# Performance work log

Hardware: AMD Instinct MI355X
Metric: run time of the kernel (lower is better)

The kernel has to match this reference:

```python
import jax, jax.numpy as jnp
import numpy as np

N = 200000   # nodes
E = 6400000  # directed edges (avg degree 32)
F = 128      # num_features
C = 16       # num_classes
H1, H2, H3 = 4, 4, 2  # hardcoded GCN hidden dims from the source


def setup_inputs():
    key = jax.random.key(0)
    ks = jax.random.split(key, 10)
    x = jax.random.normal(ks[0], (N, F), dtype=jnp.float32)
    edge_index = jax.random.randint(ks[1], (2, E), 0, N, dtype=jnp.int32)
    def lin(k, fin, fout):
        return jax.random.normal(k, (fin, fout), dtype=jnp.float32) / np.sqrt(fin).astype(np.float32)
    return {
        "x": x,
        "W1": lin(ks[2], F, H1),  "b1": jnp.zeros((H1,), jnp.float32),
        "W2": lin(ks[3], H1, H2), "b2": jnp.zeros((H2,), jnp.float32),
        "W3": lin(ks[4], H2, H3), "b3": jnp.zeros((H3,), jnp.float32),
        "Wc": lin(ks[5], H3, C),  "bc": jnp.zeros((C,), jnp.float32),
        "edge_index": edge_index,
    }


def _gcn_conv(h, W, b, src, dst, norm, n):
    # PyG GCNConv: linear first, then normalized scatter-add aggregation, then bias
    h = h @ W                                   # [n, fout]
    msg = h[src] * norm[:, None]                # gather + per-edge scale
    out = jax.ops.segment_sum(msg, dst, num_segments=n)
    return out + b


def reference(x, W1, b1, W2, b2, W3, b3, Wc, bc, edge_index):
    n = x.shape[0]
    # add self-loops (GCNConv default add_self_loops=True)
    loop = jnp.arange(n, dtype=edge_index.dtype)
    src = jnp.concatenate([edge_index[0], loop])
    dst = jnp.concatenate([edge_index[1], loop])
    # symmetric degree normalization: norm_e = deg(dst)^-1/2 * deg(src)^-1/2
    deg = jax.ops.segment_sum(jnp.ones(src.shape[0], dtype=x.dtype), dst, num_segments=n)
    dinv = jnp.where(deg > 0, jax.lax.rsqrt(deg), jnp.zeros_like(deg))
    norm = dinv[src] * dinv[dst]
    h = jnp.tanh(_gcn_conv(x, W1, b1, src, dst, norm, n))
    h = jnp.tanh(_gcn_conv(h, W2, b2, src, dst, norm, n))
    h = jnp.tanh(_gcn_conv(h, W3, b3, src, dst, norm, n))
    out = h @ Wc + bc
    return (out, h)
```

## Files before the change

kernel.cpp:

```cpp
#include <hip/hip_runtime.h>
#include <math.h>


#define NR 500
#define RNG 400
#define CAP 16384
#define HB 1024
#define EPT 8
#define EPB (HB * EPT)
#define SCAP 14336
#define Q 8
#define LROWS 32
#define LPAD 133


__global__ void k_initcur(int* __restrict__ cursor) {
    int t = blockIdx.x * blockDim.x + threadIdx.x;
    if (t < NR) cursor[t * 16] = t * CAP;
}

__global__ __launch_bounds__(HB) void k_build(const int* __restrict__ src,
                                              const int* __restrict__ dst,
                                              int* __restrict__ cursor,
                                              int* __restrict__ csrp, int e) {
    __shared__ int hist[NR];
    __shared__ int scn[HB];
    __shared__ int start[NR + 1];
    __shared__ int gbase[NR];
    __shared__ int cur[NR];
    __shared__ int buf[EPB];

    int t = threadIdx.x;
    for (int i = t; i < NR; i += HB) hist[i] = 0;
    __syncthreads();

    int ds[EPT], sr[EPT];
    int base = blockIdx.x * EPB;
#pragma unroll
    for (int k = 0; k < 2; k++) {
        int idx = base + k * HB * 4 + t * 4;
        if (idx + 3 < e) {
            int4 d4 = *(const int4*)(dst + idx);
            int4 s4 = *(const int4*)(src + idx);
            ds[4 * k + 0] = d4.x; ds[4 * k + 1] = d4.y; ds[4 * k + 2] = d4.z; ds[4 * k + 3] = d4.w;
            sr[4 * k + 0] = s4.x; sr[4 * k + 1] = s4.y; sr[4 * k + 2] = s4.z; sr[4 * k + 3] = s4.w;
        } else {
#pragma unroll
            for (int j = 0; j < 4; j++) {
                int i2 = idx + j;
                if (i2 < e) { ds[4 * k + j] = dst[i2]; sr[4 * k + j] = src[i2]; }
                else ds[4 * k + j] = -1;
            }
        }
    }
#pragma unroll
    for (int k = 0; k < EPT; k++)
        if (ds[k] >= 0) atomicAdd(&hist[ds[k] / RNG], 1);
    __syncthreads();

    scn[t] = (t < NR) ? hist[t] : 0;
    __syncthreads();
    for (int off = 1; off < HB; off <<= 1) {
        int add = (t >= off) ? scn[t - off] : 0;
        __syncthreads();
        scn[t] += add;
        __syncthreads();
    }
    if (t < NR) {
        int c = hist[t];
        int st = scn[t] - c;
        start[t] = st;
        cur[t] = st;
        gbase[t] = c ? atomicAdd(&cursor[t * 16], c) : 0;
    }
    if (t == 0) start[NR] = scn[NR - 1];
    __syncthreads();

#pragma unroll
    for (int k = 0; k < EPT; k++) {
        if (ds[k] >= 0) {
            int bin = ds[k] / RNG;
            int p = atomicAdd(&cur[bin], 1);
            buf[p] = (sr[k] << 9) | (ds[k] - bin * RNG);
        }
    }
    __syncthreads();

    int total = start[NR];
    for (int j = t; j < total; j += HB) {
        int lo = 0, hi = NR;
        while (hi - lo > 1) {
            int mid = (lo + hi) >> 1;
            if (start[mid] <= j) lo = mid; else hi = mid;
        }
        int g = gbase[lo] + (j - start[lo]);
        if (g < (lo + 1) * CAP) csrp[g] = buf[j];
    }
}


__global__ __launch_bounds__(1024) void k_sortbin(int* __restrict__ csrp,
                                                  const int* __restrict__ cursor,
                                                  float* __restrict__ dinv, int n) {
    __shared__ int deg[RNG];
    __shared__ int off[RNG];
    __shared__ int cur[RNG];
    __shared__ int sbuf[SCAP];
    int t = threadIdx.x, b = blockIdx.x;
    int s0 = b * CAP;
    int cnt = cursor[b * 16] - s0;
    if (cnt < 0) cnt = 0; if (cnt > CAP) cnt = CAP;

    for (int i = t; i < RNG; i += 1024) deg[i] = 0;
    __syncthreads();
    for (int j = t; j < cnt; j += 1024)
        atomicAdd(&deg[csrp[s0 + j] & 511], 1);
    __syncthreads();

    if (t < RNG) off[t] = deg[t];
    __syncthreads();
    for (int d = 1; d < RNG; d <<= 1) {
        int u = 0;
        if (t < RNG && t >= d) u = off[t - d];
        __syncthreads();
        if (t < RNG) off[t] += u;
        __syncthreads();
    }
    if (t < RNG) cur[t] = off[t] - deg[t];
    __syncthreads();

    for (int j = t; j < cnt; j += 1024) {
        int p = csrp[s0 + j];
        int r = atomicAdd(&cur[p & 511], 1);
        if (r < SCAP) sbuf[r] = p;
    }
    __syncthreads();
    int lim = (cnt < SCAP) ? cnt : SCAP;
    for (int j = t; j < lim; j += 1024)
        csrp[s0 + j] = sbuf[j];

    int basen = b * RNG;
    for (int i = t; i < RNG; i += 1024) {
        int node = basen + i;
        if (node < n) dinv[node] = rsqrtf(1.0f + (float)deg[i]);
    }
}


__global__ __launch_bounds__(256) void k_linear1(const float* __restrict__ x,
                                                 const float* __restrict__ W1,
                                                 const float* __restrict__ dinv,
                                                 float4* __restrict__ g1, int n) {
    __shared__ float xs[LROWS * LPAD];
    int t = threadIdx.x;
    int q = t & 7, r = t >> 3;
    int row0 = blockIdx.x * LROWS;

    float4 w[16];
#pragma unroll
    for (int i = 0; i < 16; i++) w[i] = ((const float4*)W1)[q * 16 + i];

    const float4* xg = (const float4*)(x + (size_t)row0 * 128);
    int maxI = (n - row0) * 32;
#pragma unroll
    for (int k = 0; k < 4; k++) {
        int idx = t + k * 256;
        if (idx < maxI) {
            float4 v = xg[idx];
            int rr = idx >> 5, cc = (idx & 31) << 2;
            *(float4*)&xs[rr * LPAD + cc] = v;
        }
    }
    __syncthreads();

    float p0 = 0.f, p1 = 0.f, p2 = 0.f, p3 = 0.f;
    const float* xr = &xs[r * LPAD + q * 16];
#pragma unroll
    for (int j = 0; j < 4; j++) {
        float4 xv = *(const float4*)(xr + 4 * j);
        float4 wa = w[4 * j + 0], wb = w[4 * j + 1], wc = w[4 * j + 2], wd = w[4 * j + 3];
        p0 += xv.x * wa.x + xv.y * wb.x + xv.z * wc.x + xv.w * wd.x;
        p1 += xv.x * wa.y + xv.y * wb.y + xv.z * wc.y + xv.w * wd.y;
        p2 += xv.x * wa.z + xv.y * wb.z + xv.z * wc.z + xv.w * wd.z;
        p3 += xv.x * wa.w + xv.y * wb.w + xv.z * wc.w + xv.w * wd.w;
    }
#pragma unroll
    for (int off = 1; off < 8; off <<= 1) {
        p0 += __shfl_xor(p0, off, 64);
        p1 += __shfl_xor(p1, off, 64);
        p2 += __shfl_xor(p2, off, 64);
        p3 += __shfl_xor(p3, off, 64);
    }
    int row = row0 + r;
    if (q == 0 && row < n) {
        float dv = dinv[row];
        g1[row] = make_float4(dv * p0, dv * p1, dv * p2, dv * p3);
    }
}


#define PUSH4() { qd[qc * 256 + t] = cd; \
    qv[(qc * 4 + 0) * 256 + t] = a0; qv[(qc * 4 + 1) * 256 + t] = a1; \
    qv[(qc * 4 + 2) * 256 + t] = a2; qv[(qc * 4 + 3) * 256 + t] = a3; qc++; }
#define EDGE4(di, gv) { int d_ = (di) & 511; \
    if (d_ != cd) { if (cd >= 0) PUSH4(); cd = d_; a0 = gv.x; a1 = gv.y; a2 = gv.z; a3 = gv.w; } \
    else { a0 += gv.x; a1 += gv.y; a2 += gv.z; a3 += gv.w; } }
#define FLUSH4() { for (int q = 0; q < Q; q++) { if (q < qc) { int dd = qd[q * 256 + t]; \
    atomicAdd(&acc[dd * 5 + 0], qv[(q * 4 + 0) * 256 + t]); \
    atomicAdd(&acc[dd * 5 + 1], qv[(q * 4 + 1) * 256 + t]); \
    atomicAdd(&acc[dd * 5 + 2], qv[(q * 4 + 2) * 256 + t]); \
    atomicAdd(&acc[dd * 5 + 3], qv[(q * 4 + 3) * 256 + t]); } } qc = 0; }

#define EDGELOOP4() \
    int s0 = b * CAP; \
    int cnt = cursor[b * 16] - s0; if (cnt < 0) cnt = 0; if (cnt > CAP) cnt = CAP; \
    int per = (((cnt + 255) >> 8) + 3) & ~3; \
    int lo = s0 + t * per; \
    int hi = lo + per; int eE = s0 + cnt; if (hi > eE) hi = eE; \
    int cd = -1; float a0 = 0, a1 = 0, a2 = 0, a3 = 0; \
    int qc = 0; \
    for (int j = lo; j < hi; j += 4) { \
        int4 p = *(const int4*)(csrp + j); \
        int m = hi - j; \
        int i1 = (m > 1) ? p.y : p.x; \
        int i2 = (m > 2) ? p.z : p.x; \
        int i3 = (m > 3) ? p.w : p.x; \
        float4 g0 = gin[(unsigned)p.x >> 9]; \
        float4 g1 = gin[(unsigned)i1 >> 9]; \
        float4 g2 = gin[(unsigned)i2 >> 9]; \
        float4 g3 = gin[(unsigned)i3 >> 9]; \
        EDGE4(p.x, g0); \
        if (m > 1) EDGE4(i1, g1); \
        if (m > 2) EDGE4(i2, g2); \
        if (m > 3) EDGE4(i3, g3); \
        if (__any(qc >= Q - 3)) FLUSH4(); \
    } \
    if (cd >= 0) PUSH4(); \
    FLUSH4(); \
    __syncthreads();

__global__ __launch_bounds__(256) void k_bagg44s(const int* __restrict__ csrp,
                                                 const int* __restrict__ cursor,
                                                 const float* __restrict__ dinv,
                                                 const float4* __restrict__ gin,
                                                 float4* __restrict__ gout,
                                                 const float* __restrict__ W,
                                                 const float* __restrict__ bv, int n) {
    __shared__ float acc[RNG * 5];
    __shared__ float qv[Q * 4 * 256];
    __shared__ int   qd[Q * 256];
    int t = threadIdx.x, b = blockIdx.x;
    for (int i = t; i < RNG * 5; i += 256) acc[i] = 0.0f;
    __syncthreads();
    EDGELOOP4();
    int basen = b * RNG;
    for (int i = t; i < RNG; i += 256) {
        int node = basen + i;
        if (node >= n) continue;
        float4 gs = gin[node];
        float dv = dinv[node];
        float t0 = tanhf(dv * (gs.x + acc[i * 5 + 0]) + bv[0]);
        float t1 = tanhf(dv * (gs.y + acc[i * 5 + 1]) + bv[1]);
        float t2 = tanhf(dv * (gs.z + acc[i * 5 + 2]) + bv[2]);
        float t3 = tanhf(dv * (gs.w + acc[i * 5 + 3]) + bv[3]);
        float4 o;
        o.x = dv * (t0 * W[0] + t1 * W[4] + t2 * W[8]  + t3 * W[12]);
        o.y = dv * (t0 * W[1] + t1 * W[5] + t2 * W[9]  + t3 * W[13]);
        o.z = dv * (t0 * W[2] + t1 * W[6] + t2 * W[10] + t3 * W[14]);
        o.w = dv * (t0 * W[3] + t1 * W[7] + t2 * W[11] + t3 * W[15]);
        gout[node] = o;
    }
}

__global__ __launch_bounds__(256) void k_bagg42s(const int* __restrict__ csrp,
                                                 const int* __restrict__ cursor,
                                                 const float* __restrict__ dinv,
                                                 const float4* __restrict__ gin,
                                                 float2* __restrict__ gout,
                                                 const float* __restrict__ W,
                                                 const float* __restrict__ bv, int n) {
    __shared__ float acc[RNG * 5];
    __shared__ float qv[Q * 4 * 256];
    __shared__ int   qd[Q * 256];
    int t = threadIdx.x, b = blockIdx.x;
    for (int i = t; i < RNG * 5; i += 256) acc[i] = 0.0f;
    __syncthreads();
    EDGELOOP4();
    int basen = b * RNG;
    for (int i = t; i < RNG; i += 256) {
        int node = basen + i;
        if (node >= n) continue;
        float4 gs = gin[node];
        float dv = dinv[node];
        float t0 = tanhf(dv * (gs.x + acc[i * 5 + 0]) + bv[0]);
        float t1 = tanhf(dv * (gs.y + acc[i * 5 + 1]) + bv[1]);
        float t2 = tanhf(dv * (gs.z + acc[i * 5 + 2]) + bv[2]);
        float t3 = tanhf(dv * (gs.w + acc[i * 5 + 3]) + bv[3]);
        float h0 = t0 * W[0] + t1 * W[2] + t2 * W[4] + t3 * W[6];
        float h1 = t0 * W[1] + t1 * W[3] + t2 * W[5] + t3 * W[7];
        gout[node] = make_float2(dv * h0, dv * h1);
    }
}

#define PUSH2() { qd[qc * 256 + t] = cd; \
    qv[(qc * 2 + 0) * 256 + t] = a0; qv[(qc * 2 + 1) * 256 + t] = a1; qc++; }
#define EDGE2(di, gv) { int d_ = (di) & 511; \
    if (d_ != cd) { if (cd >= 0) PUSH2(); cd = d_; a0 = gv.x; a1 = gv.y; } \
    else { a0 += gv.x; a1 += gv.y; } }
#define FLUSH2() { for (int q = 0; q < Q; q++) { if (q < qc) { int dd = qd[q * 256 + t]; \
    atomicAdd(&acc[dd * 3 + 0], qv[(q * 2 + 0) * 256 + t]); \
    atomicAdd(&acc[dd * 3 + 1], qv[(q * 2 + 1) * 256 + t]); } } qc = 0; }

__global__ __launch_bounds__(256) void k_bagg2outs(const int* __restrict__ csrp,
                                                   const int* __restrict__ cursor,
                                                   const float* __restrict__ dinv,
                                                   const float2* __restrict__ gin,
                                                   const float* __restrict__ b3,
                                                   const float* __restrict__ Wc,
                                                   const float* __restrict__ bc,
                                                   float* __restrict__ out,
                                                   float2* __restrict__ hout, int n) {
    __shared__ float acc[RNG * 3];
    __shared__ float qv[Q * 2 * 256];
    __shared__ int   qd[Q * 256];
    int t = threadIdx.x, b = blockIdx.x;
    for (int i = t; i < RNG * 3; i += 256) acc[i] = 0.0f;
    __syncthreads();
    int s0 = b * CAP;
    int cnt = cursor[b * 16] - s0; if (cnt < 0) cnt = 0; if (cnt > CAP) cnt = CAP;
    int per = (((cnt + 255) >> 8) + 3) & ~3;
    int lo = s0 + t * per;
    int hi = lo + per; int eE = s0 + cnt; if (hi > eE) hi = eE;
    int cd = -1; float a0 = 0, a1 = 0;
    int qc = 0;
    for (int j = lo; j < hi; j += 4) {
        int4 p = *(const int4*)(csrp + j);
        int m = hi - j;
        int i1 = (m > 1) ? p.y : p.x;
        int i2 = (m > 2) ? p.z : p.x;
        int i3 = (m > 3) ? p.w : p.x;
        float2 g0 = gin[(unsigned)p.x >> 9];
        float2 g1 = gin[(unsigned)i1 >> 9];
        float2 g2 = gin[(unsigned)i2 >> 9];
        float2 g3 = gin[(unsigned)i3 >> 9];
        EDGE2(p.x, g0);
        if (m > 1) EDGE2(i1, g1);
        if (m > 2) EDGE2(i2, g2);
        if (m > 3) EDGE2(i3, g3);
        if (__any(qc >= Q - 3)) FLUSH2();
    }
    if (cd >= 0) PUSH2();
    FLUSH2();
    __syncthreads();
    int basen = b * RNG;
    for (int i = t; i < RNG; i += 256) {
        int node = basen + i;
        if (node >= n) continue;
        float2 gs = gin[node];
        float dv = dinv[node];
        float t0 = tanhf(dv * (gs.x + acc[i * 3 + 0]) + b3[0]);
        float t1 = tanhf(dv * (gs.y + acc[i * 3 + 1]) + b3[1]);
        hout[node] = make_float2(t0, t1);
        float4* o = (float4*)(out + (size_t)node * 16);
#pragma unroll
        for (int q = 0; q < 4; q++) {
            float4 v;
            v.x = t0 * Wc[4 * q + 0] + t1 * Wc[16 + 4 * q + 0] + bc[4 * q + 0];
            v.y = t0 * Wc[4 * q + 1] + t1 * Wc[16 + 4 * q + 1] + bc[4 * q + 1];
            v.z = t0 * Wc[4 * q + 2] + t1 * Wc[16 + 4 * q + 2] + bc[4 * q + 2];
            v.w = t0 * Wc[4 * q + 3] + t1 * Wc[16 + 4 * q + 3] + bc[4 * q + 3];
            o[q] = v;
        }
    }
}


__global__ void k_count(const int* __restrict__ dst, int* __restrict__ cnt, int e) {
    int i = blockIdx.x * blockDim.x + threadIdx.x;
    if (i < e) atomicAdd(&cnt[dst[i]], 1);
}

__global__ void k_dinv_i(const int* __restrict__ cnt, float* __restrict__ dinv, int n) {
    int i = blockIdx.x * blockDim.x + threadIdx.x;
    if (i < n) dinv[i] = rsqrtf(1.0f + (float)cnt[i]);
}

__global__ void f_linear1(const float* __restrict__ x, const float* __restrict__ W1,
                          const float* __restrict__ dinv,
                          float* __restrict__ h, float* __restrict__ agg, int n) {
    int lane = threadIdx.x & 63;
    int wave = blockIdx.x * (blockDim.x >> 6) + (threadIdx.x >> 6);
    int nwaves = gridDim.x * (blockDim.x >> 6);
    float4 w0 = ((const float4*)W1)[2 * lane];
    float4 w1 = ((const float4*)W1)[2 * lane + 1];
    for (int row = wave; row < n; row += nwaves) {
        float2 xv = ((const float2*)(x + (size_t)row * 128))[lane];
        float p0 = xv.x * w0.x + xv.y * w1.x;
        float p1 = xv.x * w0.y + xv.y * w1.y;
        float p2 = xv.x * w0.z + xv.y * w1.z;
        float p3 = xv.x * w0.w + xv.y * w1.w;
#pragma unroll
        for (int off = 32; off; off >>= 1) {
            p0 += __shfl_xor(p0, off, 64);
            p1 += __shfl_xor(p1, off, 64);
            p2 += __shfl_xor(p2, off, 64);
            p3 += __shfl_xor(p3, off, 64);
        }
        if (lane == 0) {
            float dv = dinv[row]; float dv2 = dv * dv;
            ((float4*)h)[row] = make_float4(p0, p1, p2, p3);
            ((float4*)agg)[row] = make_float4(dv2 * p0, dv2 * p1, dv2 * p2, dv2 * p3);
        }
    }
}

__global__ void k_edge4(const int* __restrict__ src, const int* __restrict__ dst,
                        const float* __restrict__ dinv, const float* __restrict__ h,
                        float* __restrict__ agg, int e) {
    int i = blockIdx.x * blockDim.x + threadIdx.x;
    if (i >= e) return;
    int s = src[i], d = dst[i];
    float w = dinv[s] * dinv[d];
    float4 hv = ((const float4*)h)[s];
    float* a = agg + 4 * (size_t)d;
    unsafeAtomicAdd(a + 0, w * hv.x);
    unsafeAtomicAdd(a + 1, w * hv.y);
    unsafeAtomicAdd(a + 2, w * hv.z);
    unsafeAtomicAdd(a + 3, w * hv.w);
}

__global__ void k_edge2(const int* __restrict__ src, const int* __restrict__ dst,
                        const float* __restrict__ dinv, const float* __restrict__ h,
                        float* __restrict__ agg, int e) {
    int i = blockIdx.x * blockDim.x + threadIdx.x;
    if (i >= e) return;
    int s = src[i], d = dst[i];
    float w = dinv[s] * dinv[d];
    float2 hv = ((const float2*)h)[s];
    float* a = agg + 2 * (size_t)d;
    unsafeAtomicAdd(a + 0, w * hv.x);
    unsafeAtomicAdd(a + 1, w * hv.y);
}

__global__ void k_fin44(float* __restrict__ h, float* __restrict__ agg,
                        const float* __restrict__ dinv,
                        const float* __restrict__ W, const float* __restrict__ b, int n) {
    int i = blockIdx.x * blockDim.x + threadIdx.x;
    if (i >= n) return;
    float4 a = ((const float4*)agg)[i];
    float t0 = tanhf(a.x + b[0]);
    float t1 = tanhf(a.y + b[1]);
    float t2 = tanhf(a.z + b[2]);
    float t3 = tanhf(a.w + b[3]);
    float hn[4];
#pragma unroll
    for (int k = 0; k < 4; k++)
        hn[k] = t0 * W[k] + t1 * W[4 + k] + t2 * W[8 + k] + t3 * W[12 + k];
    float dv = dinv[i], dv2 = dv * dv;
    ((float4*)h)[i] = make_float4(hn[0], hn[1], hn[2], hn[3]);
    ((float4*)agg)[i] = make_float4(dv2 * hn[0], dv2 * hn[1], dv2 * hn[2], dv2 * hn[3]);
}

__global__ void k_fin42(const float* __restrict__ agg, float* __restrict__ h3,
                        float* __restrict__ agg3, const float* __restrict__ dinv,
                        const float* __restrict__ W, const float* __restrict__ b, int n) {
    int i = blockIdx.x * blockDim.x + threadIdx.x;
    if (i >= n) return;
    float4 a = ((const float4*)agg)[i];
    float t0 = tanhf(a.x + b[0]);
    float t1 = tanhf(a.y + b[1]);
    float t2 = tanhf(a.z + b[2]);
    float t3 = tanhf(a.w + b[3]);
    float h0 = t0 * W[0] + t1 * W[2] + t2 * W[4] + t3 * W[6];
    float h1 = t0 * W[1] + t1 * W[3] + t2 * W[5] + t3 * W[7];
    float dv = dinv[i], dv2 = dv * dv;
    ((float2*)h3)[i] = make_float2(h0, h1);
    ((float2*)agg3)[i] = make_float2(dv2 * h0, dv2 * h1);
}

__global__ void k_final_old(const float* __restrict__ agg3,
                            const float* __restrict__ Wc, const float* __restrict__ b3,
                            const float* __restrict__ bc,
                            float* __restrict__ out, float* __restrict__ hout, int n) {
    int i = blockIdx.x * blockDim.x + threadIdx.x;
    if (i >= n) return;
    float2 a = ((const float2*)agg3)[i];
    float t0 = tanhf(a.x + b3[0]);
    float t1 = tanhf(a.y + b3[1]);
    ((float2*)hout)[i] = make_float2(t0, t1);
    float4* o = (float4*)(out + (size_t)i * 16);
#pragma unroll
    for (int q = 0; q < 4; q++) {
        float4 v;
        v.x = t0 * Wc[4 * q + 0] + t1 * Wc[16 + 4 * q + 0] + bc[4 * q + 0];
        v.y = t0 * Wc[4 * q + 1] + t1 * Wc[16 + 4 * q + 1] + bc[4 * q + 1];
        v.z = t0 * Wc[4 * q + 2] + t1 * Wc[16 + 4 * q + 2] + bc[4 * q + 2];
        v.w = t0 * Wc[4 * q + 3] + t1 * Wc[16 + 4 * q + 3] + bc[4 * q + 3];
        o[q] = v;
    }
}


extern "C" void kernel_launch(void* const* d_in, const int* in_sizes, int n_in,
                              void* d_out, int out_size, void* d_ws, size_t ws_size,
                              hipStream_t stream) {
    const float* x   = (const float*)d_in[0];
    const float* W1  = (const float*)d_in[1];
    const float* b1  = (const float*)d_in[2];
    const float* W2  = (const float*)d_in[3];
    const float* b2  = (const float*)d_in[4];
    const float* W3  = (const float*)d_in[5];
    const float* b3  = (const float*)d_in[6];
    const float* Wc  = (const float*)d_in[7];
    const float* bc  = (const float*)d_in[8];
    const int* eidx  = (const int*)d_in[9];

    const int n = in_sizes[0] / 128;
    const int e = in_sizes[9] / 2;
    const int* src = eidx;
    const int* dst = eidx + e;

    float* out_c = (float*)d_out;
    float* out_h = (float*)d_out + 16 * (size_t)n;

    const int B = 256;
    const int gn = (n + B - 1) / B;
    const int ge = (e + B - 1) / B;
    const int nbE = (e + EPB - 1) / EPB;

    size_t nP = ((size_t)n + 3) & ~(size_t)3;

    int* csrp    = (int*)d_ws;
    int* cursor  = csrp + (size_t)NR * CAP + 4096;
    float* dinv  = (float*)(cursor + NR * 16);
    float* g1    = dinv + nP;
    float* g2    = g1 + 4 * nP;
    float* g3    = g2 + 4 * nP;
    size_t need  = (size_t)((char*)(g3 + 2 * nP) - (char*)d_ws);

    bool fast = (ws_size >= need) && (n <= NR * RNG) && (n < (1 << 18));

    if (fast) {
        k_initcur<<<(NR + 255) / 256, 256, 0, stream>>>(cursor);
        k_build<<<nbE, HB, 0, stream>>>(src, dst, cursor, csrp, e);
        k_sortbin<<<NR, 1024, 0, stream>>>(csrp, cursor, dinv, n);

        k_linear1<<<(n + LROWS - 1) / LROWS, 256, 0, stream>>>(x, W1, dinv, (float4*)g1, n);
        k_bagg44s<<<NR, 256, 0, stream>>>(csrp, cursor, dinv, (const float4*)g1,
                                          (float4*)g2, W2, b1, n);
        k_bagg42s<<<NR, 256, 0, stream>>>(csrp, cursor, dinv, (const float4*)g2,
                                          (float2*)g3, W3, b2, n);
        k_bagg2outs<<<NR, 256, 0, stream>>>(csrp, cursor, dinv, (const float2*)g3,
                                            b3, Wc, bc, out_c, (float2*)out_h, n);
    } else {
        int* fcnt   = (int*)d_ws;
        float* fdnv = (float*)d_ws + nP;
        float* h    = fdnv + nP;
        float* agg  = h + 4 * nP;
        float* h3   = agg + 4 * nP;
        float* agg3 = h3 + 2 * nP;

        hipMemsetAsync(fcnt, 0, (size_t)n * sizeof(int), stream);
        k_count<<<ge, B, 0, stream>>>(dst, fcnt, e);
        k_dinv_i<<<gn, B, 0, stream>>>(fcnt, fdnv, n);
        f_linear1<<<(n + 3) / 4, B, 0, stream>>>(x, W1, fdnv, h, agg, n);
        k_edge4<<<ge, B, 0, stream>>>(src, dst, fdnv, h, agg, e);
        k_fin44<<<gn, B, 0, stream>>>(h, agg, fdnv, W2, b1, n);
        k_edge4<<<ge, B, 0, stream>>>(src, dst, fdnv, h, agg, e);
        k_fin42<<<gn, B, 0, stream>>>(agg, h3, agg3, fdnv, W3, b2, n);
        k_edge2<<<ge, B, 0, stream>>>(src, dst, fdnv, h3, agg3, e);
        k_final_old<<<gn, B, 0, stream>>>(agg3, Wc, b3, bc, out_c, out_h, n);
    }
}
```

Measured before the change: 426.5 us.

## Halve destination bin size and software-pipeline edge gathers in aggregation

Destination bins shrink from 400 to 200 nodes, which doubles the block count (1000) and halves per-bin capacity and sort buffers. Packed edge entries now shift the source index by 8 bits instead of 9. The bucketed aggregation loops in all three layers are software-pipelined: the next group of four edge indices and their gathered features is loaded one iteration ahead, and the index vector two iterations ahead. This is meant to hide gather latency and raise parallelism, at the cost of more registers and a lower per-bin capacity. A per-bin overflow past 8192 edges would drop edges.

```diff
diff --git a/kernel.cpp b/kernel.cpp
--- a/kernel.cpp
+++ b/kernel.cpp
@@ -2,13 +2,13 @@
 #include <math.h>
 
 
-#define NR 500
-#define RNG 400
-#define CAP 16384
+#define NR 1000
+#define RNG 200
+#define CAP 8192
 #define HB 1024
 #define EPT 8
 #define EPB (HB * EPT)
-#define SCAP 14336
+#define SCAP 8192
 #define Q 8
 #define LROWS 32
 #define LPAD 133
@@ -81,7 +81,7 @@
         if (ds[k] >= 0) {
             int bin = ds[k] / RNG;
             int p = atomicAdd(&cur[bin], 1);
-            buf[p] = (sr[k] << 9) | (ds[k] - bin * RNG);
+            buf[p] = (sr[k] << 8) | (ds[k] - bin * RNG);
         }
     }
     __syncthreads();
@@ -114,7 +114,7 @@
     for (int i = t; i < RNG; i += 1024) deg[i] = 0;
     __syncthreads();
     for (int j = t; j < cnt; j += 1024)
-        atomicAdd(&deg[csrp[s0 + j] & 511], 1);
+        atomicAdd(&deg[csrp[s0 + j] & 255], 1);
     __syncthreads();
 
     if (t < RNG) off[t] = deg[t];
@@ -131,7 +131,7 @@
 
     for (int j = t; j < cnt; j += 1024) {
         int p = csrp[s0 + j];
-        int r = atomicAdd(&cur[p & 511], 1);
+        int r = atomicAdd(&cur[p & 255], 1);
         if (r < SCAP) sbuf[r] = p;
     }
     __syncthreads();
@@ -202,7 +202,7 @@
 #define PUSH4() { qd[qc * 256 + t] = cd; \
     qv[(qc * 4 + 0) * 256 + t] = a0; qv[(qc * 4 + 1) * 256 + t] = a1; \
     qv[(qc * 4 + 2) * 256 + t] = a2; qv[(qc * 4 + 3) * 256 + t] = a3; qc++; }
-#define EDGE4(di, gv) { int d_ = (di) & 511; \
+#define EDGE4(di, gv) { int d_ = (di) & 255; \
     if (d_ != cd) { if (cd >= 0) PUSH4(); cd = d_; a0 = gv.x; a1 = gv.y; a2 = gv.z; a3 = gv.w; } \
     else { a0 += gv.x; a1 += gv.y; a2 += gv.z; a3 += gv.w; } }
 #define FLUSH4() { for (int q = 0; q < Q; q++) { if (q < qc) { int dd = qd[q * 256 + t]; \
@@ -211,7 +211,7 @@
     atomicAdd(&acc[dd * 5 + 2], qv[(q * 4 + 2) * 256 + t]); \
     atomicAdd(&acc[dd * 5 + 3], qv[(q * 4 + 3) * 256 + t]); } } qc = 0; }
 
-#define EDGELOOP4() \
+#define EDGELOOP4P() \
     int s0 = b * CAP; \
     int cnt = cursor[b * 16] - s0; if (cnt < 0) cnt = 0; if (cnt > CAP) cnt = CAP; \
     int per = (((cnt + 255) >> 8) + 3) & ~3; \
@@ -219,16 +219,38 @@
     int hi = lo + per; int eE = s0 + cnt; if (hi > eE) hi = eE; \
     int cd = -1; float a0 = 0, a1 = 0, a2 = 0, a3 = 0; \
     int qc = 0; \
+    int4 pA, pB; \
+    float4 gA0, gA1, gA2, gA3; \
+    if (lo < hi) { \
+        pA = *(const int4*)(csrp + lo); \
+        int mA = hi - lo; \
+        int e1 = (mA > 1) ? pA.y : pA.x; \
+        int e2 = (mA > 2) ? pA.z : pA.x; \
+        int e3 = (mA > 3) ? pA.w : pA.x; \
+        gA0 = gin[(unsigned)pA.x >> 8]; gA1 = gin[(unsigned)e1 >> 8]; \
+        gA2 = gin[(unsigned)e2 >> 8]; gA3 = gin[(unsigned)e3 >> 8]; \
+        int jB = lo + 4; \
+        pB = *(const int4*)(csrp + ((jB < hi) ? jB : lo)); \
+    } \
     for (int j = lo; j < hi; j += 4) { \
-        int4 p = *(const int4*)(csrp + j); \
+        int4 p = pA; \
+        float4 g0 = gA0, g1 = gA1, g2 = gA2, g3 = gA3; \
         int m = hi - j; \
+        int jn = j + 4; \
+        pA = pB; \
+        if (jn < hi) { \
+            int mN = hi - jn; \
+            int e1 = (mN > 1) ? pA.y : pA.x; \
+            int e2 = (mN > 2) ? pA.z : pA.x; \
+            int e3 = (mN > 3) ? pA.w : pA.x; \
+            gA0 = gin[(unsigned)pA.x >> 8]; gA1 = gin[(unsigned)e1 >> 8]; \
+            gA2 = gin[(unsigned)e2 >> 8]; gA3 = gin[(unsigned)e3 >> 8]; \
+        } \
+        int jB2 = j + 8; \
+        pB = *(const int4*)(csrp + ((jB2 < hi) ? jB2 : lo)); \
         int i1 = (m > 1) ? p.y : p.x; \
         int i2 = (m > 2) ? p.z : p.x; \
         int i3 = (m > 3) ? p.w : p.x; \
-        float4 g0 = gin[(unsigned)p.x >> 9]; \
-        float4 g1 = gin[(unsigned)i1 >> 9]; \
-        float4 g2 = gin[(unsigned)i2 >> 9]; \
-        float4 g3 = gin[(unsigned)i3 >> 9]; \
         EDGE4(p.x, g0); \
         if (m > 1) EDGE4(i1, g1); \
         if (m > 2) EDGE4(i2, g2); \
@@ -252,7 +274,7 @@
     int t = threadIdx.x, b = blockIdx.x;
     for (int i = t; i < RNG * 5; i += 256) acc[i] = 0.0f;
     __syncthreads();
-    EDGELOOP4();
+    EDGELOOP4P();
     int basen = b * RNG;
     for (int i = t; i < RNG; i += 256) {
         int node = basen + i;
@@ -285,7 +307,7 @@
     int t = threadIdx.x, b = blockIdx.x;
     for (int i = t; i < RNG * 5; i += 256) acc[i] = 0.0f;
     __syncthreads();
-    EDGELOOP4();
+    EDGELOOP4P();
     int basen = b * RNG;
     for (int i = t; i < RNG; i += 256) {
         int node = basen + i;
@@ -304,7 +326,7 @@
 
 #define PUSH2() { qd[qc * 256 + t] = cd; \
     qv[(qc * 2 + 0) * 256 + t] = a0; qv[(qc * 2 + 1) * 256 + t] = a1; qc++; }
-#define EDGE2(di, gv) { int d_ = (di) & 511; \
+#define EDGE2(di, gv) { int d_ = (di) & 255; \
     if (d_ != cd) { if (cd >= 0) PUSH2(); cd = d_; a0 = gv.x; a1 = gv.y; } \
     else { a0 += gv.x; a1 += gv.y; } }
 #define FLUSH2() { for (int q = 0; q < Q; q++) { if (q < qc) { int dd = qd[q * 256 + t]; \
@@ -333,16 +355,38 @@
     int hi = lo + per; int eE = s0 + cnt; if (hi > eE) hi = eE;
     int cd = -1; float a0 = 0, a1 = 0;
     int qc = 0;
+    int4 pA, pB;
+    float2 gA0, gA1, gA2, gA3;
+    if (lo < hi) {
+        pA = *(const int4*)(csrp + lo);
+        int mA = hi - lo;
+        int e1 = (mA > 1) ? pA.y : pA.x;
+        int e2 = (mA > 2) ? pA.z : pA.x;
+        int e3 = (mA > 3) ? pA.w : pA.x;
+        gA0 = gin[(unsigned)pA.x >> 8]; gA1 = gin[(unsigned)e1 >> 8];
+        gA2 = gin[(unsigned)e2 >> 8]; gA3 = gin[(unsigned)e3 >> 8];
+        int jB = lo + 4;
+        pB = *(const int4*)(csrp + ((jB < hi) ? jB : lo));
+    }
     for (int j = lo; j < hi; j += 4) {
-        int4 p = *(const int4*)(csrp + j);
+        int4 p = pA;
+        float2 g0 = gA0, g1 = gA1, g2 = gA2, g3 = gA3;
         int m = hi - j;
+        int jn = j + 4;
+        pA = pB;
+        if (jn < hi) {
+            int mN = hi - jn;
+            int e1 = (mN > 1) ? pA.y : pA.x;
+            int e2 = (mN > 2) ? pA.z : pA.x;
+            int e3 = (mN > 3) ? pA.w : pA.x;
+            gA0 = gin[(unsigned)pA.x >> 8]; gA1 = gin[(unsigned)e1 >> 8];
+            gA2 = gin[(unsigned)e2 >> 8]; gA3 = gin[(unsigned)e3 >> 8];
+        }
+        int jB2 = j + 8;
+        pB = *(const int4*)(csrp + ((jB2 < hi) ? jB2 : lo));
         int i1 = (m > 1) ? p.y : p.x;
         int i2 = (m > 2) ? p.z : p.x;
         int i3 = (m > 3) ? p.w : p.x;
-        float2 g0 = gin[(unsigned)p.x >> 9];
-        float2 g1 = gin[(unsigned)i1 >> 9];
-        float2 g2 = gin[(unsigned)i2 >> 9];
-        float2 g3 = gin[(unsigned)i3 >> 9];
         EDGE2(p.x, g0);
         if (m > 1) EDGE2(i1, g1);
         if (m > 2) EDGE2(i2, g2);
@@ -569,6 +613,6 @@
         k_edge4<<<ge, B, 0, stream>>>(src, dst, fdnv, h, agg, e);
         k_fin42<<<gn, B, 0, stream>>>(agg, h3, agg3, fdnv, W3, b2, n);
         k_edge2<<<ge, B, 0, stream>>>(src, dst, fdnv, h3, agg3, e);
-        k_final_old<<<gn, B, 0, stream>>>(agg3, Wc, b3, bc, out_c, out_h, n);
-    }
-}
+        k_final_old<<<gn, B, 0, stream>>>(agg3, Wc, b3, bc, out_c, (float*)out_h, n);
+    }
+}
```

Result: no change. 422.7 us (-0.9%).
